# Kernel tuning notes

Measured on AMD Instinct MI355X. Metric: run time of the kernel, lower is better.

Reference implementation:

```python
import jax, jax.numpy as jnp
import numpy as np

IN_DIM, HID, MEM, OUT = 512, 1024, 1024, 512
BATCH = 4096
HIST = 5  # hist_steps hard-coded in MMU.__init__

_LINEARS = [("inpgate", IN_DIM, HID), ("rec_inpgate", OUT, HID), ("mem_inpgate", MEM, HID),
            ("inp", IN_DIM, HID), ("rec_inp", OUT, HID),
            ("readgate", IN_DIM, MEM), ("rec_readgate", OUT, MEM), ("mem_readgate", MEM, MEM),
            ("decoder", HID, MEM),
            ("writegate", IN_DIM, MEM), ("rec_writegate", OUT, MEM), ("mem_writegate", MEM, MEM),
            ("encoder", MEM, HID)]


def setup_inputs() -> dict:
    key = jax.random.key(0)
    ks = iter(jax.random.split(key, 2 * len(_LINEARS) + 4))
    d = {"input": jax.random.normal(next(ks), (IN_DIM, BATCH), jnp.float32)}
    for name, fin, fout in _LINEARS:
        bound = 1.0 / np.sqrt(fin)  # torch nn.Linear default init range
        d["W_" + name] = jax.random.uniform(next(ks), (fout, fin), jnp.float32, -bound, bound)
        d["b_" + name] = jax.random.uniform(next(ks), (fout,), jnp.float32, -bound, bound)
    d["w_hid_out"] = jax.random.uniform(next(ks), (OUT, MEM), jnp.float32)  # torch.rand
    return d


def reference(input, W_inpgate, b_inpgate, W_rec_inpgate, b_rec_inpgate,
              W_mem_inpgate, b_mem_inpgate, W_inp, b_inp, W_rec_inp, b_rec_inp,
              W_readgate, b_readgate, W_rec_readgate, b_rec_readgate,
              W_mem_readgate, b_mem_readgate, W_decoder, b_decoder,
              W_writegate, b_writegate, W_rec_writegate, b_rec_writegate,
              W_mem_writegate, b_mem_writegate, W_encoder, b_encoder, w_hid_out):
    B = input.shape[1]
    lin = lambda x, W, b: x @ W.T + b
    # fresh module: history is zeros except last slot = current input (transposed to [B, in])
    xs = jnp.concatenate([jnp.zeros((HIST - 1, B, IN_DIM), input.dtype), input.T[None]], axis=0)

    def step(carry, x):
        out, mem = carry  # [B, OUT], [B, MEM]
        block_inp = jax.nn.sigmoid(lin(x, W_inp, b_inp) + lin(out, W_rec_inp, b_rec_inp))
        inp_gate = jax.nn.sigmoid(lin(x, W_inpgate, b_inpgate) + lin(mem, W_mem_inpgate, b_mem_inpgate)
                                  + lin(out, W_rec_inpgate, b_rec_inpgate))
        read_gate = jax.nn.sigmoid(lin(x, W_readgate, b_readgate) + lin(mem, W_mem_readgate, b_mem_readgate)
                                   + lin(out, W_rec_readgate, b_rec_readgate))
        decoded_mem = lin(read_gate * mem, W_decoder, b_decoder)
        hidden = decoded_mem + block_inp * inp_gate  # [B, HID] (HID == MEM)
        write_gate = jax.nn.sigmoid(lin(x, W_writegate, b_writegate) + lin(mem, W_mem_writegate, b_mem_writegate)
                                    + lin(out, W_rec_writegate, b_rec_writegate))
        encoded = jnp.tanh(lin(hidden, W_encoder, b_encoder))
        mem = (1.0 - write_gate) * mem + write_gate * encoded
        out = hidden @ w_hid_out.T  # w_hid_out.mm(hidden.T).T
        return (out, mem), None

    init = (jnp.zeros((B, OUT), input.dtype), jnp.zeros((B, MEM), input.dtype))
    (out, _mem), _ = jax.lax.scan(step, init, xs)
    return out
```

## Files before the change

kernel.cpp:

```cpp
#include <hip/hip_runtime.h>
#include <hip/hip_bf16.h>
#include <math.h>

typedef __hip_bfloat16 bf16;
typedef __attribute__((ext_vector_type(8))) short s16x8;
typedef __attribute__((ext_vector_type(4))) float f32x4;

__device__ __forceinline__ float fsig(float x) {
  return __builtin_amdgcn_rcpf(1.0f + __expf(-x));
}
__device__ __forceinline__ float ftanh(float x) { return 2.0f * fsig(2.0f * x) - 1.0f; }
__device__ __forceinline__ float dot4(float4 a, float4 b) {
  return a.x * b.x + a.y * b.y + a.z * b.z + a.w * b.w;
}
__device__ __forceinline__ float wred(float s) {
#pragma unroll
  for (int off = 32; off > 0; off >>= 1) s += __shfl_down(s, off, 64);
  return s;
}

__global__ void setup(const float* __restrict__ W_inp, const float* __restrict__ W_ig,
                      const float* __restrict__ W_rg, const float* __restrict__ W_ho,
                      const float* __restrict__ W_dec, const float* __restrict__ W_enc,
                      const float* __restrict__ input,
                      const float* __restrict__ b_inp, const float* __restrict__ b_rinp,
                      const float* __restrict__ b_ig, const float* __restrict__ b_mig,
                      const float* __restrict__ b_rig, const float* __restrict__ b_wg,
                      const float* __restrict__ b_mwg, const float* __restrict__ b_rwg,
                      const float* __restrict__ b_dec, bf16* __restrict__ Wcat,
                      bf16* __restrict__ WhoB, bf16* __restrict__ Wcat2, bf16* __restrict__ Wdt,
                      bf16* __restrict__ WencB, bf16* __restrict__ Xb,
                      float* __restrict__ out_s, float* __restrict__ mem_s,
                      float* __restrict__ hidv, float* __restrict__ wgv,
                      float* __restrict__ vout, float* __restrict__ Web) {
  __shared__ float t[32][33];
  const int id = blockIdx.x, tid = threadIdx.x;
  if (id < 12294) {
    const int i = id * 256 + tid;
    if (i < 524288) {
      Wcat[i] = __float2bfloat16(W_inp[i]);
    } else if (i < 1048576) {
      Wcat[i] = __float2bfloat16(W_ig[i - 524288]);
    } else if (i < 1572864) {
      Wcat[i] = __float2bfloat16(W_rg[i - 1048576]);
    } else if (i < 2097152) {
      const int k = i - 1572864;
      const bf16 vv = __float2bfloat16(W_ho[k]);
      WhoB[k] = vv;
      Wcat2[(size_t)(k >> 10) * 2048 + (k & 1023)] = vv;
    } else if (i < 2098688) {
      const int tt = i - 2097152;
      if (tt < 512) out_s[tt] = 0.0f;
      else mem_s[tt - 512] = 0.0f;
    } else if (i < 3147264) {
      const int k = i - 2098688;
      WencB[k] = __float2bfloat16(W_enc[k]);
    }
  } else if (id < 14342) {
    const int b = id - 12294;
    const int i0 = (b >> 7) * 32, b0 = (b & 127) * 32;
    const int tx = tid & 31, ty = tid >> 5;
#pragma unroll
    for (int r = ty; r < 32; r += 8) t[r][tx] = input[(size_t)(i0 + r) * 4096 + b0 + tx];
    __syncthreads();
#pragma unroll
    for (int r = ty; r < 32; r += 8)
      Xb[(size_t)(b0 + r) * 512 + i0 + tx] = __float2bfloat16(t[tx][r]);
  } else if (id < 15366) {
    const int b = id - 14342;
    const int j0 = (b >> 5) * 32, k0 = (b & 31) * 32;
    const int tx = tid & 31, ty = tid >> 5;
#pragma unroll
    for (int r = ty; r < 32; r += 8) t[r][tx] = W_dec[(size_t)(j0 + r) * 1024 + k0 + tx];
    __syncthreads();
#pragma unroll
    for (int r = ty; r < 32; r += 8)
      Wdt[(size_t)(k0 + r) * 1024 + j0 + tx] = __float2bfloat16(t[tx][r]);
  } else if (id < 15370) {
    const int j = (id - 15366) * 256 + tid;
    const float bi = fsig(b_inp[j] + b_rinp[j]);
    const float ig = fsig(b_ig[j] + b_mig[j] + b_rig[j]);
    hidv[j] = b_dec[j] + bi * ig;
    wgv[j] = fsig(b_wg[j] + b_mwg[j] + b_rwg[j]);
  } else {
    const int o = id - 15370;
    const float* row = (o < 512) ? (W_ho + (size_t)o * 1024) : (W_enc + (size_t)(o - 512) * 1024);
    const float4 a = *(const float4*)(row + tid * 4);
    const float4 b = *(const float4*)(b_dec + tid * 4);
    float s = wred(dot4(a, b));
    if ((tid & 63) == 0) t[0][tid >> 6] = s;
    __syncthreads();
    if (tid == 0) {
      const float d = t[0][0] + t[0][1] + t[0][2] + t[0][3];
      if (o < 512) vout[o] = d;
      else Web[o - 512] = d;
    }
  }
}

__global__ void step_gates(const float* __restrict__ Wri, const float* __restrict__ Wmig,
                           const float* __restrict__ Wrig, const float* __restrict__ Wmrg,
                           const float* __restrict__ Wrrg, const float* __restrict__ Wmwg,
                           const float* __restrict__ Wrwg, const float* __restrict__ b_inp,
                           const float* __restrict__ b_rinp, const float* __restrict__ b_ig,
                           const float* __restrict__ b_mig, const float* __restrict__ b_rig,
                           const float* __restrict__ b_rg, const float* __restrict__ b_mrg,
                           const float* __restrict__ b_rrg, const float* __restrict__ b_wg,
                           const float* __restrict__ b_mwg, const float* __restrict__ b_rwg,
                           const float* __restrict__ out_s, const float* __restrict__ mem_s,
                           float* __restrict__ rgm, float* __restrict__ h0v,
                           float* __restrict__ wgv) {
  __shared__ float red[7][4];
  const int j = blockIdx.x, tid = threadIdx.x, lane = tid & 63, wave = tid >> 6;
  const float4 z = make_float4(0.f, 0.f, 0.f, 0.f);
  const float4 o4 = (tid < 128) ? *(const float4*)(out_s + tid * 4) : z;
  const float4 m4 = *(const float4*)(mem_s + tid * 4);
  float p[7];
  p[0] = dot4((tid < 128) ? *(const float4*)(Wri + (size_t)j * 512 + tid * 4) : z, o4);
  p[1] = dot4(*(const float4*)(Wmig + (size_t)j * 1024 + tid * 4), m4);
  p[2] = dot4((tid < 128) ? *(const float4*)(Wrig + (size_t)j * 512 + tid * 4) : z, o4);
  p[3] = dot4(*(const float4*)(Wmrg + (size_t)j * 1024 + tid * 4), m4);
  p[4] = dot4((tid < 128) ? *(const float4*)(Wrrg + (size_t)j * 512 + tid * 4) : z, o4);
  p[5] = dot4(*(const float4*)(Wmwg + (size_t)j * 1024 + tid * 4), m4);
  p[6] = dot4((tid < 128) ? *(const float4*)(Wrwg + (size_t)j * 512 + tid * 4) : z, o4);
#pragma unroll
  for (int d = 0; d < 7; ++d) {
    float s = wred(p[d]);
    if (lane == 0) red[d][wave] = s;
  }
  __syncthreads();
  if (tid == 0) {
    float D[7];
#pragma unroll
    for (int d = 0; d < 7; ++d) D[d] = red[d][0] + red[d][1] + red[d][2] + red[d][3];
    const float abi = b_inp[j] + b_rinp[j] + D[0];
    const float aig = b_ig[j] + b_mig[j] + b_rig[j] + D[1] + D[2];
    const float arg = b_rg[j] + b_mrg[j] + b_rrg[j] + D[3] + D[4];
    const float awg = b_wg[j] + b_mwg[j] + b_rwg[j] + D[5] + D[6];
    rgm[j] = fsig(arg) * mem_s[j];
    h0v[j] = fsig(abi) * fsig(aig);
    wgv[j] = fsig(awg);
  }
}

__global__ void step_fuse(const float* __restrict__ E, const float* __restrict__ Wenc,
                          const float* __restrict__ P, const float* __restrict__ Who,
                          const float* __restrict__ b_enc, const float* __restrict__ Web,
                          const float* __restrict__ vout, const float* __restrict__ rgm,
                          const float* __restrict__ h0v, const float* __restrict__ wgv,
                          float* __restrict__ mem_s, float* __restrict__ out_s) {
  __shared__ float red[4];
  const int id = blockIdx.x, tid = threadIdx.x;
  const float4 r4 = *(const float4*)(rgm + tid * 4);
  const float4 h4 = *(const float4*)(h0v + tid * 4);
  const float* Ar = (id < 1024) ? (E + (size_t)id * 1024) : (P + (size_t)(id - 1024) * 1024);
  const float* Br = (id < 1024) ? (Wenc + (size_t)id * 1024) : (Who + (size_t)(id - 1024) * 1024);
  const float s1 = dot4(*(const float4*)(Ar + tid * 4), r4);
  const float s2 = dot4(*(const float4*)(Br + tid * 4), h4);
  const float s = wred(s1 + s2);
  if ((tid & 63) == 0) red[tid >> 6] = s;
  __syncthreads();
  if (tid == 0) {
    const float d = red[0] + red[1] + red[2] + red[3];
    if (id < 1024) {
      const float wg = wgv[id];
      mem_s[id] = (1.0f - wg) * mem_s[id] + wg * ftanh(b_enc[id] + Web[id] + d);
    } else {
      out_s[id - 1024] = vout[id - 1024] + d;
    }
  }
}

__global__ __launch_bounds__(256) void update0_pe(
    const float* __restrict__ Wenc, const float* __restrict__ b_enc,
    const float* __restrict__ Who, const float* __restrict__ hidv,
    const float* __restrict__ wgv, float* __restrict__ mem_s, float* __restrict__ out_s,
    const bf16* __restrict__ WhoB, const bf16* __restrict__ WencB,
    const bf16* __restrict__ Wdt, float* __restrict__ P, float* __restrict__ E) {
  __shared__ char smem[16384];
  const int tid = threadIdx.x;
  if (blockIdx.x < 1536) {
    float* red = (float*)smem;
    const int id = blockIdx.x;
    const float* row =
        (id < 1024) ? (Wenc + (size_t)id * 1024) : (Who + (size_t)(id - 1024) * 1024);
    const float4 a = *(const float4*)(row + tid * 4);
    const float4 b = *(const float4*)(hidv + tid * 4);
    float s = wred(dot4(a, b));
    if ((tid & 63) == 0) red[tid >> 6] = s;
    __syncthreads();
    if (tid == 0) {
      const float d = red[0] + red[1] + red[2] + red[3];
      if (id < 1024) {
        const float wg = wgv[id];
        mem_s[id] = (1.0f - wg) * mem_s[id] + wg * ftanh(b_enc[id] + d);
      } else {
        out_s[id - 1024] = d;
      }
    }
    return;
  }
  const int bi = blockIdx.x - 1536;
  const bf16* Ag;
  float* Cg;
  int m0, n0, kt0;
  if (bi < 256) {
    Ag = WhoB; Cg = P;
    m0 = ((bi >> 4) & 7) * 64; n0 = (bi & 15) * 64; kt0 = (bi >> 7) * 512;
  } else {
    const int b2 = bi - 256;
    Ag = WencB; Cg = E;
    m0 = ((b2 >> 4) & 15) * 64; n0 = (b2 & 15) * 64; kt0 = (b2 >> 8) * 512;
  }
  const int wave = tid >> 6, lane = tid & 63;
  const int wm = wave >> 1, wn = wave & 1;
  f32x4 acc[2][2] = {};
  for (int kt = kt0; kt < kt0 + 512; kt += 64) {
    __syncthreads();
#pragma unroll
    for (int i = 0; i < 2; ++i) {
      const int ci = i * 256 + tid;
      const int row = ci >> 3, ck = (ci & 7) ^ (row & 7);
      const bf16* g = Ag + (size_t)(m0 + row) * 1024 + kt + ck * 8;
      const unsigned lofs = (unsigned)__builtin_amdgcn_readfirstlane((i * 256 + wave * 64) * 16);
      __builtin_amdgcn_global_load_lds(
          (const __attribute__((address_space(1))) void*)g,
          (__attribute__((address_space(3))) void*)(smem + lofs), 16, 0, 0);
    }
#pragma unroll
    for (int i = 0; i < 2; ++i) {
      const int ci = i * 256 + tid;
      const int row = ci >> 3, ck = (ci & 7) ^ (row & 7);
      const bf16* g = Wdt + (size_t)(n0 + row) * 1024 + kt + ck * 8;
      const unsigned lofs =
          (unsigned)__builtin_amdgcn_readfirstlane(8192 + (i * 256 + wave * 64) * 16);
      __builtin_amdgcn_global_load_lds(
          (const __attribute__((address_space(1))) void*)g,
          (__attribute__((address_space(3))) void*)(smem + lofs), 16, 0, 0);
    }
    __syncthreads();
#pragma unroll
    for (int ks = 0; ks < 2; ++ks) {
      const int ckk = ks * 4 + (lane >> 4);
      s16x8 af[2];
#pragma unroll
      for (int i = 0; i < 2; ++i) {
        const int R = wm * 32 + i * 16 + (lane & 15);
        af[i] = *(const s16x8*)(smem + (R * 8 + (ckk ^ (R & 7))) * 16);
      }
#pragma unroll
      for (int j = 0; j < 2; ++j) {
        const int R = wn * 32 + j * 16 + (lane & 15);
        const s16x8 bfr = *(const s16x8*)(smem + 8192 + (R * 8 + (ckk ^ (R & 7))) * 16);
#pragma unroll
        for (int i = 0; i < 2; ++i)
          acc[i][j] = __builtin_amdgcn_mfma_f32_16x16x32_bf16(af[i], bfr, acc[i][j], 0, 0, 0);
      }
    }
  }
  const int mb = (lane >> 4) * 4, nb = lane & 15;
#pragma unroll
  for (int i = 0; i < 2; ++i) {
#pragma unroll
    for (int j = 0; j < 2; ++j) {
      const int col = n0 + wn * 32 + j * 16 + nb;
#pragma unroll
      for (int r = 0; r < 4; ++r) {
        const int rowg = m0 + wm * 32 + i * 16 + mb + r;
        atomicAdd(Cg + (size_t)rowg * 1024 + col, acc[i][j][r]);
      }
    }
  }
}

__global__ void final_consts(const float* __restrict__ Wri, const float* __restrict__ Wmig,
                             const float* __restrict__ Wrig, const float* __restrict__ Wmrg,
                             const float* __restrict__ Wrrg, const float* __restrict__ b_inp,
                             const float* __restrict__ b_rinp, const float* __restrict__ b_ig,
                             const float* __restrict__ b_mig, const float* __restrict__ b_rig,
                             const float* __restrict__ b_rg, const float* __restrict__ b_mrg,
                             const float* __restrict__ b_rrg, const float* __restrict__ out_s,
                             const float* __restrict__ mem_s, const float* __restrict__ P,
                             float* __restrict__ ccat, bf16* __restrict__ Wcat2) {
  __shared__ float red[5][4];
  const int id = blockIdx.x, tid = threadIdx.x, lane = tid & 63, wave = tid >> 6;
  if (id < 1024) {
    const float4 z = make_float4(0.f, 0.f, 0.f, 0.f);
    const float4 o4 = (tid < 128) ? *(const float4*)(out_s + tid * 4) : z;
    const float4 m4 = *(const float4*)(mem_s + tid * 4);
    float p[5];
    p[0] = dot4((tid < 128) ? *(const float4*)(Wri + (size_t)id * 512 + tid * 4) : z, o4);
    p[1] = dot4(*(const float4*)(Wmig + (size_t)id * 1024 + tid * 4), m4);
    p[2] = dot4((tid < 128) ? *(const float4*)(Wrig + (size_t)id * 512 + tid * 4) : z, o4);
    p[3] = dot4(*(const float4*)(Wmrg + (size_t)id * 1024 + tid * 4), m4);
    p[4] = dot4((tid < 128) ? *(const float4*)(Wrrg + (size_t)id * 512 + tid * 4) : z, o4);
#pragma unroll
    for (int d = 0; d < 5; ++d) {
      float s = wred(p[d]);
      if (lane == 0) red[d][wave] = s;
    }
    __syncthreads();
    if (tid == 0) {
      float D[5];
#pragma unroll
      for (int d = 0; d < 5; ++d) D[d] = red[d][0] + red[d][1] + red[d][2] + red[d][3];
      ccat[id] = b_inp[id] + b_rinp[id] + D[0];
      ccat[1024 + id] = b_ig[id] + b_mig[id] + b_rig[id] + D[1] + D[2];
      ccat[2048 + id] = b_rg[id] + b_mrg[id] + b_rrg[id] + D[3] + D[4];
    }
  } else {
    const int idx = (id - 1024) * 256 + tid;
    const int q = idx >> 10, k = idx & 1023;
    Wcat2[(size_t)q * 2048 + 1024 + k] = __float2bfloat16(P[idx] * mem_s[k]);
  }
}

__global__ __launch_bounds__(256, 4) void gemm_gates(const bf16* __restrict__ A,
                                                     const bf16* __restrict__ Wcat,
                                                     const float* __restrict__ ccat,
                                                     bf16* __restrict__ Hcat) {
  __shared__ char smem[32768];
  const int tid = threadIdx.x, wave = tid >> 6, lane = tid & 63;
  const int wm = wave >> 1, wn = wave & 1;
  const int m0 = blockIdx.y * 64, n0 = blockIdx.x * 64;
  f32x4 acc[3][2][2] = {};

  for (int kt = 0; kt < 512; kt += 64) {
    __syncthreads();
#pragma unroll
    for (int i = 0; i < 2; ++i) {
      const int ci = i * 256 + tid;
      const int row = ci >> 3, ck = (ci & 7) ^ (row & 7);
      const bf16* g = A + (size_t)(m0 + row) * 512 + kt + ck * 8;
      const unsigned lofs = (unsigned)__builtin_amdgcn_readfirstlane((i * 256 + wave * 64) * 16);
      __builtin_amdgcn_global_load_lds(
          (const __attribute__((address_space(1))) void*)g,
          (__attribute__((address_space(3))) void*)(smem + lofs), 16, 0, 0);
    }
#pragma unroll
    for (int gI = 0; gI < 3; ++gI) {
      const bf16* Bp = Wcat + gI * 524288;
#pragma unroll
      for (int i = 0; i < 2; ++i) {
        const int ci = i * 256 + tid;
        const int row = ci >> 3, ck = (ci & 7) ^ (row & 7);
        const bf16* g = Bp + (size_t)(n0 + row) * 512 + kt + ck * 8;
        const unsigned lofs = (unsigned)__builtin_amdgcn_readfirstlane(
            8192 + gI * 8192 + (i * 256 + wave * 64) * 16);
        __builtin_amdgcn_global_load_lds(
            (const __attribute__((address_space(1))) void*)g,
            (__attribute__((address_space(3))) void*)(smem + lofs), 16, 0, 0);
      }
    }
    __syncthreads();

#pragma unroll
    for (int ks = 0; ks < 2; ++ks) {
      const int ckk = ks * 4 + (lane >> 4);
      s16x8 af[2];
#pragma unroll
      for (int i = 0; i < 2; ++i) {
        const int R = wm * 32 + i * 16 + (lane & 15);
        af[i] = *(const s16x8*)(smem + (R * 8 + (ckk ^ (R & 7))) * 16);
      }
#pragma unroll
      for (int gI = 0; gI < 3; ++gI) {
#pragma unroll
        for (int j = 0; j < 2; ++j) {
          const int R = wn * 32 + j * 16 + (lane & 15);
          const s16x8 bfr =
              *(const s16x8*)(smem + 8192 + gI * 8192 + (R * 8 + (ckk ^ (R & 7))) * 16);
#pragma unroll
          for (int i = 0; i < 2; ++i)
            acc[gI][i][j] =
                __builtin_amdgcn_mfma_f32_16x16x32_bf16(af[i], bfr, acc[gI][i][j], 0, 0, 0);
        }
      }
    }
  }

  __syncthreads();
  bf16* sm = (bf16*)smem;
  bf16* sr = (bf16*)smem + 5120;
  const int mb = (lane >> 4) * 4, nb = lane & 15;
#pragma unroll
  for (int i = 0; i < 2; ++i) {
#pragma unroll
    for (int j = 0; j < 2; ++j) {
      const int colL = wn * 32 + j * 16 + nb;
      const int jg = n0 + colL;
      const float c0 = ccat[jg], c1 = ccat[1024 + jg], c2 = ccat[2048 + jg];
#pragma unroll
      for (int r = 0; r < 4; ++r) {
        const int rowL = wm * 32 + i * 16 + mb + r;
        const float h = fsig(acc[0][i][j][r] + c0) * fsig(acc[1][i][j][r] + c1);
        const float rg = fsig(acc[2][i][j][r] + c2);
        sm[rowL * 80 + colL] = __float2bfloat16(h);
        sr[rowL * 80 + colL] = __float2bfloat16(rg);
      }
    }
  }
  __syncthreads();
#pragma unroll
  for (int pp = 0; pp < 2; ++pp) {
    const int c = pp * 256 + tid;
    const int row = c >> 3, cc = c & 7;
    const s16x8 v0 = *(const s16x8*)(sm + row * 80 + cc * 8);
    const s16x8 v1 = *(const s16x8*)(sr + row * 80 + cc * 8);
    *(s16x8*)(Hcat + (size_t)(m0 + row) * 2048 + n0 + cc * 8) = v0;
    *(s16x8*)(Hcat + (size_t)(m0 + row) * 2048 + 1024 + n0 + cc * 8) = v1;
  }
}

__global__ __launch_bounds__(256, 4) void gemm_out(const bf16* __restrict__ A,
                                                   const bf16* __restrict__ Bp,
                                                   const float* __restrict__ vout,
                                                   float* __restrict__ outF) {
  __shared__ char smem[16384];
  const int tid = threadIdx.x, wave = tid >> 6, lane = tid & 63;
  const int wm = wave >> 1, wn = wave & 1;
  const int m0 = blockIdx.y * 64, n0 = blockIdx.x * 64;
  f32x4 acc[2][2] = {};

  for (int kt = 0; kt < 2048; kt += 64) {
    __syncthreads();
#pragma unroll
    for (int i = 0; i < 2; ++i) {
      const int ci = i * 256 + tid;
      const int row = ci >> 3, ck = (ci & 7) ^ (row & 7);
      const bf16* g = A + (size_t)(m0 + row) * 2048 + kt + ck * 8;
      const unsigned lofs = (unsigned)__builtin_amdgcn_readfirstlane((i * 256 + wave * 64) * 16);
      __builtin_amdgcn_global_load_lds(
          (const __attribute__((address_space(1))) void*)g,
          (__attribute__((address_space(3))) void*)(smem + lofs), 16, 0, 0);
    }
#pragma unroll
    for (int i = 0; i < 2; ++i) {
      const int ci = i * 256 + tid;
      const int row = ci >> 3, ck = (ci & 7) ^ (row & 7);
      const bf16* g = Bp + (size_t)(n0 + row) * 2048 + kt + ck * 8;
      const unsigned lofs =
          (unsigned)__builtin_amdgcn_readfirstlane(8192 + (i * 256 + wave * 64) * 16);
      __builtin_amdgcn_global_load_lds(
          (const __attribute__((address_space(1))) void*)g,
          (__attribute__((address_space(3))) void*)(smem + lofs), 16, 0, 0);
    }
    __syncthreads();

#pragma unroll
    for (int ks = 0; ks < 2; ++ks) {
      const int ckk = ks * 4 + (lane >> 4);
      s16x8 af[2];
#pragma unroll
      for (int i = 0; i < 2; ++i) {
        const int R = wm * 32 + i * 16 + (lane & 15);
        af[i] = *(const s16x8*)(smem + (R * 8 + (ckk ^ (R & 7))) * 16);
      }
#pragma unroll
      for (int j = 0; j < 2; ++j) {
        const int R = wn * 32 + j * 16 + (lane & 15);
        const s16x8 bfr = *(const s16x8*)(smem + 8192 + (R * 8 + (ckk ^ (R & 7))) * 16);
#pragma unroll
        for (int i = 0; i < 2; ++i)
          acc[i][j] = __builtin_amdgcn_mfma_f32_16x16x32_bf16(af[i], bfr, acc[i][j], 0, 0, 0);
      }
    }
  }

  const int mb = (lane >> 4) * 4, nb = lane & 15;
#pragma unroll
  for (int i = 0; i < 2; ++i) {
#pragma unroll
    for (int j = 0; j < 2; ++j) {
      const int col = n0 + wn * 32 + j * 16 + nb;
#pragma unroll
      for (int r = 0; r < 4; ++r) {
        const int rowg = m0 + wm * 32 + i * 16 + mb + r;
        outF[(size_t)rowg * 512 + col] = acc[i][j][r] + vout[col];
      }
    }
  }
}

extern "C" void kernel_launch(void* const* d_in, const int* in_sizes, int n_in, void* d_out,
                              int out_size, void* d_ws, size_t ws_size, hipStream_t stream) {
  const float* input  = (const float*)d_in[0];
  const float* W_ig   = (const float*)d_in[1];  const float* b_ig   = (const float*)d_in[2];
  const float* W_rig  = (const float*)d_in[3];  const float* b_rig  = (const float*)d_in[4];
  const float* W_mig  = (const float*)d_in[5];  const float* b_mig  = (const float*)d_in[6];
  const float* W_inp  = (const float*)d_in[7];  const float* b_inp  = (const float*)d_in[8];
  const float* W_rinp = (const float*)d_in[9];  const float* b_rinp = (const float*)d_in[10];
  const float* W_rg   = (const float*)d_in[11]; const float* b_rg   = (const float*)d_in[12];
  const float* W_rrg  = (const float*)d_in[13]; const float* b_rrg  = (const float*)d_in[14];
  const float* W_mrg  = (const float*)d_in[15]; const float* b_mrg  = (const float*)d_in[16];
  const float* W_dec  = (const float*)d_in[17]; const float* b_dec  = (const float*)d_in[18];
  const float* W_wg   = (const float*)d_in[19]; const float* b_wg   = (const float*)d_in[20];
  const float* W_rwg  = (const float*)d_in[21]; const float* b_rwg  = (const float*)d_in[22];
  const float* W_mwg  = (const float*)d_in[23]; const float* b_mwg  = (const float*)d_in[24];
  const float* W_enc  = (const float*)d_in[25]; const float* b_enc  = (const float*)d_in[26];
  const float* W_ho   = (const float*)d_in[27];
  (void)W_wg;

  char* ws = (char*)d_ws;
  float* out_s = (float*)(ws + 0);
  float* mem_s = (float*)(ws + 4096);
  float* rgm   = (float*)(ws + 8192);
  float* h0v   = (float*)(ws + 12288);
  float* wgv   = (float*)(ws + 16384);
  float* hidv  = (float*)(ws + 20480);
  float* ccat  = (float*)(ws + 24576);
  float* vout  = (float*)(ws + 40960);
  float* Web   = (float*)(ws + 45056);
  float* P     = (float*)(ws + 65536);
  bf16* Xb     = (bf16*)(ws + 2162688);
  bf16* Wcat   = (bf16*)(ws + 6356992);
  bf16* WhoB   = (bf16*)(ws + 9502720);
  bf16* Wcat2  = (bf16*)(ws + 10551296);
  bf16* Wdt    = (bf16*)(ws + 12648448);
  bf16* Hcat   = (bf16*)(ws + 14745600);
  float* E     = (float*)(ws + 31522816);
  bf16* WencB  = (bf16*)(ws + 35717120);

  setup<<<16906, 256, 0, stream>>>(W_inp, W_ig, W_rg, W_ho, W_dec, W_enc, input, b_inp, b_rinp,
                                   b_ig, b_mig, b_rig, b_wg, b_mwg, b_rwg, b_dec, Wcat, WhoB,
                                   Wcat2, Wdt, WencB, Xb, out_s, mem_s, hidv, wgv, vout, Web);

  update0_pe<<<2304, 256, 0, stream>>>(W_enc, b_enc, W_ho, hidv, wgv, mem_s, out_s, WhoB, WencB,
                                       Wdt, P, E);

  for (int s = 0; s < 3; ++s) {
    step_gates<<<1024, 256, 0, stream>>>(W_rinp, W_mig, W_rig, W_mrg, W_rrg, W_mwg, W_rwg, b_inp,
                                         b_rinp, b_ig, b_mig, b_rig, b_rg, b_mrg, b_rrg, b_wg,
                                         b_mwg, b_rwg, out_s, mem_s, rgm, h0v, wgv);
    step_fuse<<<1536, 256, 0, stream>>>(E, W_enc, P, W_ho, b_enc, Web, vout, rgm, h0v, wgv,
                                        mem_s, out_s);
  }

  final_consts<<<3072, 256, 0, stream>>>(W_rinp, W_mig, W_rig, W_mrg, W_rrg, b_inp, b_rinp, b_ig,
                                         b_mig, b_rig, b_rg, b_mrg, b_rrg, out_s, mem_s, P, ccat,
                                         Wcat2);

  gemm_gates<<<dim3(16, 64), 256, 0, stream>>>(Xb, Wcat, ccat, Hcat);

  gemm_out<<<dim3(8, 64), 256, 0, stream>>>(Hcat, Wcat2, vout, (float*)d_out);
}
```

Measured before the change: 229.8 us.

## Fold first-step update into setup and overlap P/E GEMM with step gates

The first recurrent step's update, which depends only on biases because the initial state is zero, now runs inside the setup kernel as extra blocks instead of a separate update0_pe launch. The bf16 P/E precompute GEMM blocks now launch together with the first step_gates pass in one combined gates_pe kernel. This drops one kernel launch and lets the GEMM overlap the gate dot products. It relies on the zero initial state: the old out_s/mem_s zeroing is removed and mem_s is written directly.

```diff
diff --git a/kernel.cpp b/kernel.cpp
--- a/kernel.cpp
+++ b/kernel.cpp
@@ -27,15 +27,15 @@
                       const float* __restrict__ b_ig, const float* __restrict__ b_mig,
                       const float* __restrict__ b_rig, const float* __restrict__ b_wg,
                       const float* __restrict__ b_mwg, const float* __restrict__ b_rwg,
-                      const float* __restrict__ b_dec, bf16* __restrict__ Wcat,
+                      const float* __restrict__ b_dec, const float* __restrict__ b_enc,
+                      bf16* __restrict__ Wcat,
                       bf16* __restrict__ WhoB, bf16* __restrict__ Wcat2, bf16* __restrict__ Wdt,
                       bf16* __restrict__ WencB, bf16* __restrict__ Xb,
                       float* __restrict__ out_s, float* __restrict__ mem_s,
-                      float* __restrict__ hidv, float* __restrict__ wgv,
                       float* __restrict__ vout, float* __restrict__ Web) {
   __shared__ float t[32][33];
   const int id = blockIdx.x, tid = threadIdx.x;
-  if (id < 12294) {
+  if (id < 12288) {
     const int i = id * 256 + tid;
     if (i < 524288) {
       Wcat[i] = __float2bfloat16(W_inp[i]);
@@ -48,16 +48,12 @@
       const bf16 vv = __float2bfloat16(W_ho[k]);
       WhoB[k] = vv;
       Wcat2[(size_t)(k >> 10) * 2048 + (k & 1023)] = vv;
-    } else if (i < 2098688) {
-      const int tt = i - 2097152;
-      if (tt < 512) out_s[tt] = 0.0f;
-      else mem_s[tt - 512] = 0.0f;
-    } else if (i < 3147264) {
-      const int k = i - 2098688;
+    } else {
+      const int k = i - 2097152;
       WencB[k] = __float2bfloat16(W_enc[k]);
     }
-  } else if (id < 14342) {
-    const int b = id - 12294;
+  } else if (id < 14336) {
+    const int b = id - 12288;
     const int i0 = (b >> 7) * 32, b0 = (b & 127) * 32;
     const int tx = tid & 31, ty = tid >> 5;
 #pragma unroll
@@ -66,8 +62,8 @@
 #pragma unroll
     for (int r = ty; r < 32; r += 8)
       Xb[(size_t)(b0 + r) * 512 + i0 + tx] = __float2bfloat16(t[tx][r]);
-  } else if (id < 15366) {
-    const int b = id - 14342;
+  } else if (id < 15360) {
+    const int b = id - 14336;
     const int j0 = (b >> 5) * 32, k0 = (b & 31) * 32;
     const int tx = tid & 31, ty = tid >> 5;
 #pragma unroll
@@ -76,14 +72,8 @@
 #pragma unroll
     for (int r = ty; r < 32; r += 8)
       Wdt[(size_t)(k0 + r) * 1024 + j0 + tx] = __float2bfloat16(t[tx][r]);
-  } else if (id < 15370) {
-    const int j = (id - 15366) * 256 + tid;
-    const float bi = fsig(b_inp[j] + b_rinp[j]);
-    const float ig = fsig(b_ig[j] + b_mig[j] + b_rig[j]);
-    hidv[j] = b_dec[j] + bi * ig;
-    wgv[j] = fsig(b_wg[j] + b_mwg[j] + b_rwg[j]);
-  } else {
-    const int o = id - 15370;
+  } else if (id < 16896) {
+    const int o = id - 15360;
     const float* row = (o < 512) ? (W_ho + (size_t)o * 1024) : (W_enc + (size_t)(o - 512) * 1024);
     const float4 a = *(const float4*)(row + tid * 4);
     const float4 b = *(const float4*)(b_dec + tid * 4);
@@ -95,51 +85,157 @@
       if (o < 512) vout[o] = d;
       else Web[o - 512] = d;
     }
-  }
-}
-
-__global__ void step_gates(const float* __restrict__ Wri, const float* __restrict__ Wmig,
-                           const float* __restrict__ Wrig, const float* __restrict__ Wmrg,
-                           const float* __restrict__ Wrrg, const float* __restrict__ Wmwg,
-                           const float* __restrict__ Wrwg, const float* __restrict__ b_inp,
-                           const float* __restrict__ b_rinp, const float* __restrict__ b_ig,
-                           const float* __restrict__ b_mig, const float* __restrict__ b_rig,
-                           const float* __restrict__ b_rg, const float* __restrict__ b_mrg,
-                           const float* __restrict__ b_rrg, const float* __restrict__ b_wg,
-                           const float* __restrict__ b_mwg, const float* __restrict__ b_rwg,
-                           const float* __restrict__ out_s, const float* __restrict__ mem_s,
-                           float* __restrict__ rgm, float* __restrict__ h0v,
-                           float* __restrict__ wgv) {
-  __shared__ float red[7][4];
-  const int j = blockIdx.x, tid = threadIdx.x, lane = tid & 63, wave = tid >> 6;
-  const float4 z = make_float4(0.f, 0.f, 0.f, 0.f);
-  const float4 o4 = (tid < 128) ? *(const float4*)(out_s + tid * 4) : z;
-  const float4 m4 = *(const float4*)(mem_s + tid * 4);
-  float p[7];
-  p[0] = dot4((tid < 128) ? *(const float4*)(Wri + (size_t)j * 512 + tid * 4) : z, o4);
-  p[1] = dot4(*(const float4*)(Wmig + (size_t)j * 1024 + tid * 4), m4);
-  p[2] = dot4((tid < 128) ? *(const float4*)(Wrig + (size_t)j * 512 + tid * 4) : z, o4);
-  p[3] = dot4(*(const float4*)(Wmrg + (size_t)j * 1024 + tid * 4), m4);
-  p[4] = dot4((tid < 128) ? *(const float4*)(Wrrg + (size_t)j * 512 + tid * 4) : z, o4);
-  p[5] = dot4(*(const float4*)(Wmwg + (size_t)j * 1024 + tid * 4), m4);
-  p[6] = dot4((tid < 128) ? *(const float4*)(Wrwg + (size_t)j * 512 + tid * 4) : z, o4);
-#pragma unroll
-  for (int d = 0; d < 7; ++d) {
-    float s = wred(p[d]);
-    if (lane == 0) red[d][wave] = s;
-  }
-  __syncthreads();
-  if (tid == 0) {
-    float D[7];
-#pragma unroll
-    for (int d = 0; d < 7; ++d) D[d] = red[d][0] + red[d][1] + red[d][2] + red[d][3];
-    const float abi = b_inp[j] + b_rinp[j] + D[0];
-    const float aig = b_ig[j] + b_mig[j] + b_rig[j] + D[1] + D[2];
-    const float arg = b_rg[j] + b_mrg[j] + b_rrg[j] + D[3] + D[4];
-    const float awg = b_wg[j] + b_mwg[j] + b_rwg[j] + D[5] + D[6];
-    rgm[j] = fsig(arg) * mem_s[j];
-    h0v[j] = fsig(abi) * fsig(aig);
-    wgv[j] = fsig(awg);
+  } else {
+    const int id2 = id - 16896;
+    const float4 bd = *(const float4*)(b_dec + tid * 4);
+    const float4 v1 = *(const float4*)(b_inp + tid * 4);
+    const float4 v2 = *(const float4*)(b_rinp + tid * 4);
+    const float4 v3 = *(const float4*)(b_ig + tid * 4);
+    const float4 v4 = *(const float4*)(b_mig + tid * 4);
+    const float4 v5 = *(const float4*)(b_rig + tid * 4);
+    float4 hv;
+    hv.x = bd.x + fsig(v1.x + v2.x) * fsig(v3.x + v4.x + v5.x);
+    hv.y = bd.y + fsig(v1.y + v2.y) * fsig(v3.y + v4.y + v5.y);
+    hv.z = bd.z + fsig(v1.z + v2.z) * fsig(v3.z + v4.z + v5.z);
+    hv.w = bd.w + fsig(v1.w + v2.w) * fsig(v3.w + v4.w + v5.w);
+    const float* row =
+        (id2 < 1024) ? (W_enc + (size_t)id2 * 1024) : (W_ho + (size_t)(id2 - 1024) * 1024);
+    float s = wred(dot4(*(const float4*)(row + tid * 4), hv));
+    if ((tid & 63) == 0) t[0][tid >> 6] = s;
+    __syncthreads();
+    if (tid == 0) {
+      const float d = t[0][0] + t[0][1] + t[0][2] + t[0][3];
+      if (id2 < 1024) {
+        const float wg = fsig(b_wg[id2] + b_mwg[id2] + b_rwg[id2]);
+        mem_s[id2] = wg * ftanh(b_enc[id2] + d);
+      } else {
+        out_s[id2 - 1024] = d;
+      }
+    }
+  }
+}
+
+__global__ __launch_bounds__(256) void gates_pe(
+    const float* __restrict__ Wri, const float* __restrict__ Wmig,
+    const float* __restrict__ Wrig, const float* __restrict__ Wmrg,
+    const float* __restrict__ Wrrg, const float* __restrict__ Wmwg,
+    const float* __restrict__ Wrwg, const float* __restrict__ b_inp,
+    const float* __restrict__ b_rinp, const float* __restrict__ b_ig,
+    const float* __restrict__ b_mig, const float* __restrict__ b_rig,
+    const float* __restrict__ b_rg, const float* __restrict__ b_mrg,
+    const float* __restrict__ b_rrg, const float* __restrict__ b_wg,
+    const float* __restrict__ b_mwg, const float* __restrict__ b_rwg,
+    const float* __restrict__ out_s, const float* __restrict__ mem_s,
+    float* __restrict__ rgm, float* __restrict__ h0v, float* __restrict__ wgv,
+    const bf16* __restrict__ WhoB, const bf16* __restrict__ WencB,
+    const bf16* __restrict__ Wdt, float* __restrict__ P, float* __restrict__ E,
+    int pe_blocks) {
+  __shared__ char smem[16384];
+  const int tid = threadIdx.x;
+  if ((int)blockIdx.x >= pe_blocks) {
+    float(*red)[4] = (float(*)[4])smem;
+    const int j = blockIdx.x - pe_blocks, lane = tid & 63, wave = tid >> 6;
+    const float4 z = make_float4(0.f, 0.f, 0.f, 0.f);
+    const float4 o4 = (tid < 128) ? *(const float4*)(out_s + tid * 4) : z;
+    const float4 m4 = *(const float4*)(mem_s + tid * 4);
+    float p[7];
+    p[0] = dot4((tid < 128) ? *(const float4*)(Wri + (size_t)j * 512 + tid * 4) : z, o4);
+    p[1] = dot4(*(const float4*)(Wmig + (size_t)j * 1024 + tid * 4), m4);
+    p[2] = dot4((tid < 128) ? *(const float4*)(Wrig + (size_t)j * 512 + tid * 4) : z, o4);
+    p[3] = dot4(*(const float4*)(Wmrg + (size_t)j * 1024 + tid * 4), m4);
+    p[4] = dot4((tid < 128) ? *(const float4*)(Wrrg + (size_t)j * 512 + tid * 4) : z, o4);
+    p[5] = dot4(*(const float4*)(Wmwg + (size_t)j * 1024 + tid * 4), m4);
+    p[6] = dot4((tid < 128) ? *(const float4*)(Wrwg + (size_t)j * 512 + tid * 4) : z, o4);
+#pragma unroll
+    for (int d = 0; d < 7; ++d) {
+      float s = wred(p[d]);
+      if (lane == 0) red[d][wave] = s;
+    }
+    __syncthreads();
+    if (tid == 0) {
+      float D[7];
+#pragma unroll
+      for (int d = 0; d < 7; ++d) D[d] = red[d][0] + red[d][1] + red[d][2] + red[d][3];
+      const float abi = b_inp[j] + b_rinp[j] + D[0];
+      const float aig = b_ig[j] + b_mig[j] + b_rig[j] + D[1] + D[2];
+      const float arg = b_rg[j] + b_mrg[j] + b_rrg[j] + D[3] + D[4];
+      const float awg = b_wg[j] + b_mwg[j] + b_rwg[j] + D[5] + D[6];
+      rgm[j] = fsig(arg) * mem_s[j];
+      h0v[j] = fsig(abi) * fsig(aig);
+      wgv[j] = fsig(awg);
+    }
+    return;
+  }
+  const int bi = blockIdx.x;
+  const bf16* Ag;
+  float* Cg;
+  int m0, n0, kt0;
+  if (bi < 256) {
+    Ag = WhoB; Cg = P;
+    m0 = ((bi >> 4) & 7) * 64; n0 = (bi & 15) * 64; kt0 = (bi >> 7) * 512;
+  } else {
+    const int b2 = bi - 256;
+    Ag = WencB; Cg = E;
+    m0 = ((b2 >> 4) & 15) * 64; n0 = (b2 & 15) * 64; kt0 = (b2 >> 8) * 512;
+  }
+  const int wave = tid >> 6, lane = tid & 63;
+  const int wm = wave >> 1, wn = wave & 1;
+  f32x4 acc[2][2] = {};
+  for (int kt = kt0; kt < kt0 + 512; kt += 64) {
+    __syncthreads();
+#pragma unroll
+    for (int i = 0; i < 2; ++i) {
+      const int ci = i * 256 + tid;
+      const int row = ci >> 3, ck = (ci & 7) ^ (row & 7);
+      const bf16* g = Ag + (size_t)(m0 + row) * 1024 + kt + ck * 8;
+      const unsigned lofs = (unsigned)__builtin_amdgcn_readfirstlane((i * 256 + wave * 64) * 16);
+      __builtin_amdgcn_global_load_lds(
+          (const __attribute__((address_space(1))) void*)g,
+          (__attribute__((address_space(3))) void*)(smem + lofs), 16, 0, 0);
+    }
+#pragma unroll
+    for (int i = 0; i < 2; ++i) {
+      const int ci = i * 256 + tid;
+      const int row = ci >> 3, ck = (ci & 7) ^ (row & 7);
+      const bf16* g = Wdt + (size_t)(n0 + row) * 1024 + kt + ck * 8;
+      const unsigned lofs =
+          (unsigned)__builtin_amdgcn_readfirstlane(8192 + (i * 256 + wave * 64) * 16);
+      __builtin_amdgcn_global_load_lds(
+          (const __attribute__((address_space(1))) void*)g,
+          (__attribute__((address_space(3))) void*)(smem + lofs), 16, 0, 0);
+    }
+    __syncthreads();
+#pragma unroll
+    for (int ks = 0; ks < 2; ++ks) {
+      const int ckk = ks * 4 + (lane >> 4);
+      s16x8 af[2];
+#pragma unroll
+      for (int i = 0; i < 2; ++i) {
+        const int R = wm * 32 + i * 16 + (lane & 15);
+        af[i] = *(const s16x8*)(smem + (R * 8 + (ckk ^ (R & 7))) * 16);
+      }
+#pragma unroll
+      for (int j = 0; j < 2; ++j) {
+        const int R = wn * 32 + j * 16 + (lane & 15);
+        const s16x8 bfr = *(const s16x8*)(smem + 8192 + (R * 8 + (ckk ^ (R & 7))) * 16);
+#pragma unroll
+        for (int i = 0; i < 2; ++i)
+          acc[i][j] = __builtin_amdgcn_mfma_f32_16x16x32_bf16(af[i], bfr, acc[i][j], 0, 0, 0);
+      }
+    }
+  }
+  const int mb = (lane >> 4) * 4, nb = lane & 15;
+#pragma unroll
+  for (int i = 0; i < 2; ++i) {
+#pragma unroll
+    for (int j = 0; j < 2; ++j) {
+      const int col = n0 + wn * 32 + j * 16 + nb;
+#pragma unroll
+      for (int r = 0; r < 4; ++r) {
+        const int rowg = m0 + wm * 32 + i * 16 + mb + r;
+        atomicAdd(Cg + (size_t)rowg * 1024 + col, acc[i][j][r]);
+      }
+    }
   }
 }
 
@@ -171,108 +267,6 @@
   }
 }
 
-__global__ __launch_bounds__(256) void update0_pe(
-    const float* __restrict__ Wenc, const float* __restrict__ b_enc,
-    const float* __restrict__ Who, const float* __restrict__ hidv,
-    const float* __restrict__ wgv, float* __restrict__ mem_s, float* __restrict__ out_s,
-    const bf16* __restrict__ WhoB, const bf16* __restrict__ WencB,
-    const bf16* __restrict__ Wdt, float* __restrict__ P, float* __restrict__ E) {
-  __shared__ char smem[16384];
-  const int tid = threadIdx.x;
-  if (blockIdx.x < 1536) {
-    float* red = (float*)smem;
-    const int id = blockIdx.x;
-    const float* row =
-        (id < 1024) ? (Wenc + (size_t)id * 1024) : (Who + (size_t)(id - 1024) * 1024);
-    const float4 a = *(const float4*)(row + tid * 4);
-    const float4 b = *(const float4*)(hidv + tid * 4);
-    float s = wred(dot4(a, b));
-    if ((tid & 63) == 0) red[tid >> 6] = s;
-    __syncthreads();
-    if (tid == 0) {
-      const float d = red[0] + red[1] + red[2] + red[3];
-      if (id < 1024) {
-        const float wg = wgv[id];
-        mem_s[id] = (1.0f - wg) * mem_s[id] + wg * ftanh(b_enc[id] + d);
-      } else {
-        out_s[id - 1024] = d;
-      }
-    }
-    return;
-  }
-  const int bi = blockIdx.x - 1536;
-  const bf16* Ag;
-  float* Cg;
-  int m0, n0, kt0;
-  if (bi < 256) {
-    Ag = WhoB; Cg = P;
-    m0 = ((bi >> 4) & 7) * 64; n0 = (bi & 15) * 64; kt0 = (bi >> 7) * 512;
-  } else {
-    const int b2 = bi - 256;
-    Ag = WencB; Cg = E;
-    m0 = ((b2 >> 4) & 15) * 64; n0 = (b2 & 15) * 64; kt0 = (b2 >> 8) * 512;
-  }
-  const int wave = tid >> 6, lane = tid & 63;
-  const int wm = wave >> 1, wn = wave & 1;
-  f32x4 acc[2][2] = {};
-  for (int kt = kt0; kt < kt0 + 512; kt += 64) {
-    __syncthreads();
-#pragma unroll
-    for (int i = 0; i < 2; ++i) {
-      const int ci = i * 256 + tid;
-      const int row = ci >> 3, ck = (ci & 7) ^ (row & 7);
-      const bf16* g = Ag + (size_t)(m0 + row) * 1024 + kt + ck * 8;
-      const unsigned lofs = (unsigned)__builtin_amdgcn_readfirstlane((i * 256 + wave * 64) * 16);
-      __builtin_amdgcn_global_load_lds(
-          (const __attribute__((address_space(1))) void*)g,
-          (__attribute__((address_space(3))) void*)(smem + lofs), 16, 0, 0);
-    }
-#pragma unroll
-    for (int i = 0; i < 2; ++i) {
-      const int ci = i * 256 + tid;
-      const int row = ci >> 3, ck = (ci & 7) ^ (row & 7);
-      const bf16* g = Wdt + (size_t)(n0 + row) * 1024 + kt + ck * 8;
-      const unsigned lofs =
-          (unsigned)__builtin_amdgcn_readfirstlane(8192 + (i * 256 + wave * 64) * 16);
-      __builtin_amdgcn_global_load_lds(
-          (const __attribute__((address_space(1))) void*)g,
-          (__attribute__((address_space(3))) void*)(smem + lofs), 16, 0, 0);
-    }
-    __syncthreads();
-#pragma unroll
-    for (int ks = 0; ks < 2; ++ks) {
-      const int ckk = ks * 4 + (lane >> 4);
-      s16x8 af[2];
-#pragma unroll
-      for (int i = 0; i < 2; ++i) {
-        const int R = wm * 32 + i * 16 + (lane & 15);
-        af[i] = *(const s16x8*)(smem + (R * 8 + (ckk ^ (R & 7))) * 16);
-      }
-#pragma unroll
-      for (int j = 0; j < 2; ++j) {
-        const int R = wn * 32 + j * 16 + (lane & 15);
-        const s16x8 bfr = *(const s16x8*)(smem + 8192 + (R * 8 + (ckk ^ (R & 7))) * 16);
-#pragma unroll
-        for (int i = 0; i < 2; ++i)
-          acc[i][j] = __builtin_amdgcn_mfma_f32_16x16x32_bf16(af[i], bfr, acc[i][j], 0, 0, 0);
-      }
-    }
-  }
-  const int mb = (lane >> 4) * 4, nb = lane & 15;
-#pragma unroll
-  for (int i = 0; i < 2; ++i) {
-#pragma unroll
-    for (int j = 0; j < 2; ++j) {
-      const int col = n0 + wn * 32 + j * 16 + nb;
-#pragma unroll
-      for (int r = 0; r < 4; ++r) {
-        const int rowg = m0 + wm * 32 + i * 16 + mb + r;
-        atomicAdd(Cg + (size_t)rowg * 1024 + col, acc[i][j][r]);
-      }
-    }
-  }
-}
-
 __global__ void final_consts(const float* __restrict__ Wri, const float* __restrict__ Wmig,
                              const float* __restrict__ Wrig, const float* __restrict__ Wmrg,
                              const float* __restrict__ Wrrg, const float* __restrict__ b_inp,
@@ -507,7 +501,6 @@
   float* rgm   = (float*)(ws + 8192);
   float* h0v   = (float*)(ws + 12288);
   float* wgv   = (float*)(ws + 16384);
-  float* hidv  = (float*)(ws + 20480);
   float* ccat  = (float*)(ws + 24576);
   float* vout  = (float*)(ws + 40960);
   float* Web   = (float*)(ws + 45056);
@@ -521,17 +514,16 @@
   float* E     = (float*)(ws + 31522816);
   bf16* WencB  = (bf16*)(ws + 35717120);
 
-  setup<<<16906, 256, 0, stream>>>(W_inp, W_ig, W_rg, W_ho, W_dec, W_enc, input, b_inp, b_rinp,
-                                   b_ig, b_mig, b_rig, b_wg, b_mwg, b_rwg, b_dec, Wcat, WhoB,
-                                   Wcat2, Wdt, WencB, Xb, out_s, mem_s, hidv, wgv, vout, Web);
-
-  update0_pe<<<2304, 256, 0, stream>>>(W_enc, b_enc, W_ho, hidv, wgv, mem_s, out_s, WhoB, WencB,
-                                       Wdt, P, E);
+  setup<<<18432, 256, 0, stream>>>(W_inp, W_ig, W_rg, W_ho, W_dec, W_enc, input, b_inp, b_rinp,
+                                   b_ig, b_mig, b_rig, b_wg, b_mwg, b_rwg, b_dec, b_enc, Wcat,
+                                   WhoB, Wcat2, Wdt, WencB, Xb, out_s, mem_s, vout, Web);
 
   for (int s = 0; s < 3; ++s) {
-    step_gates<<<1024, 256, 0, stream>>>(W_rinp, W_mig, W_rig, W_mrg, W_rrg, W_mwg, W_rwg, b_inp,
-                                         b_rinp, b_ig, b_mig, b_rig, b_rg, b_mrg, b_rrg, b_wg,
-                                         b_mwg, b_rwg, out_s, mem_s, rgm, h0v, wgv);
+    const int pe = (s == 0) ? 768 : 0;
+    gates_pe<<<1024 + pe, 256, 0, stream>>>(W_rinp, W_mig, W_rig, W_mrg, W_rrg, W_mwg, W_rwg,
+                                            b_inp, b_rinp, b_ig, b_mig, b_rig, b_rg, b_mrg,
+                                            b_rrg, b_wg, b_mwg, b_rwg, out_s, mem_s, rgm, h0v,
+                                            wgv, WhoB, WencB, Wdt, P, E, pe);
     step_fuse<<<1536, 256, 0, stream>>>(E, W_enc, P, W_ho, b_enc, Web, vout, rgm, h0v, wgv,
                                         mem_s, out_s);
   }
```

Result: no change. 227.7 us (-0.9%).
